# Performance work log

Measured on AMD Instinct MI355X. Metric: run time of the kernel, lower is better.

The kernel has to match this reference:

```python
import jax, jax.numpy as jnp
import numpy as np
from jax import lax


def conv2d(x, w, b, stride=1, pad=1):
    y = lax.conv_general_dilated(x, w, (stride, stride), [(pad, pad), (pad, pad)],
                                 dimension_numbers=('NCHW', 'OIHW', 'NCHW'))
    return y + b[None, :, None, None]


def nearest_resize(x, H, W):
    # torch F.interpolate(mode='nearest'): src = floor(dst * in / out)
    h, w = x.shape[-2:]
    iy = (jnp.arange(H) * h) // H
    ix = (jnp.arange(W) * w) // W
    return x[:, :, iy[:, None], ix[None, :]]


def deform_conv2d(x, offset, w, b):
    # torchvision DeformConv2d: kernel 3x3, stride 1, pad 1, dilation 1, 1 offset group
    B, C, H, W = x.shape
    K = 9
    off = offset.reshape(B, K, 2, H, W)  # per kernel tap: (dy, dx)
    dy = (jnp.arange(K) // 3 - 1).astype(x.dtype)
    dx = (jnp.arange(K) % 3 - 1).astype(x.dtype)
    yy = jnp.arange(H, dtype=x.dtype)[None, None, :, None]
    xx = jnp.arange(W, dtype=x.dtype)[None, None, None, :]
    py = yy + dy[None, :, None, None] + off[:, :, 0]  # [B,K,H,W] sample rows
    px = xx + dx[None, :, None, None] + off[:, :, 1]  # [B,K,H,W] sample cols
    y0 = jnp.floor(py)
    x0 = jnp.floor(px)
    ly = py - y0
    lx = px - x0
    y0i = y0.astype(jnp.int32)
    x0i = x0.astype(jnp.int32)
    x_flat = x.reshape(B, C, H * W)

    def gather(yi, xi, wgt):
        # zero contribution for out-of-bounds corners (torchvision zero padding)
        valid = (yi >= 0) & (yi < H) & (xi >= 0) & (xi < W)
        idx = (jnp.clip(yi, 0, H - 1) * W + jnp.clip(xi, 0, W - 1)).reshape(B, -1)
        vals = jax.vmap(lambda xf, i: xf[:, i])(x_flat, idx)  # [B, C, K*H*W]
        wv = (wgt * valid.astype(x.dtype)).reshape(B, 1, -1)
        return vals * wv

    s = gather(y0i, x0i, (1 - ly) * (1 - lx))
    s = s + gather(y0i, x0i + 1, (1 - ly) * lx)
    s = s + gather(y0i + 1, x0i, ly * (1 - lx))
    s = s + gather(y0i + 1, x0i + 1, ly * lx)
    s = s.reshape(B, C, K, H * W)  # bilinear-sampled taps
    O = w.shape[0]
    out = jnp.einsum('bckn,ock->bon', s, w.reshape(O, C, K))
    return out.reshape(B, O, H, W) + b[None, :, None, None]


def setup_inputs() -> dict:
    key = jax.random.key(0)
    ks = jax.random.split(key, 12)
    B, Ccnn, H, W = 8, 768, 28, 28
    Cvit, hv, wv = 3840, 14, 14
    d_hidn, Cout = 512, 768

    def he(k, shape):
        fan_in = shape[1] * shape[2] * shape[3]
        return jax.random.normal(k, shape, jnp.float32) * np.float32(np.sqrt(2.0 / fan_in))

    return {
        'cnn_feat': jax.random.normal(ks[0], (B, Ccnn, H, W), jnp.float32),
        'vit_feat': jax.random.normal(ks[1], (B, Cvit, hv, wv), jnp.float32),
        'w_off': he(ks[2], (18, Cvit, 3, 3)),
        'b_off': jnp.zeros((18,), jnp.float32),
        'w_def': he(ks[3], (Cout, Ccnn, 3, 3)),
        'b_def': jax.random.normal(ks[4], (Cout,), jnp.float32) * 0.01,
        'w1': he(ks[5], (d_hidn, Cout, 3, 3)),
        'b1': jax.random.normal(ks[6], (d_hidn,), jnp.float32) * 0.01,
        'w2': he(ks[7], (Cout, d_hidn, 3, 3)),
        'b2': jax.random.normal(ks[8], (Cout,), jnp.float32) * 0.01,
    }


def reference(cnn_feat, vit_feat, w_off, b_off, w_def, b_def, w1, b1, w2, b2):
    H, W = cnn_feat.shape[-2:]
    v = nearest_resize(vit_feat, H, W)
    offset = conv2d(v, w_off, b_off)                 # [B,18,H,W]
    d = deform_conv2d(cnn_feat, offset, w_def, b_def)  # [B,768,H,W]
    h = jax.nn.relu(conv2d(d, w1, b1, stride=2))     # [B,512,H/2,W/2]
    return conv2d(h, w2, b2, stride=1)               # [B,768,H/2,W/2]
```

## Files before the change

kernel.cpp:

```cpp
#include <hip/hip_runtime.h>
#include <hip/hip_bf16.h>
#include <stdint.h>

typedef __attribute__((ext_vector_type(8))) short v8s;
typedef __attribute__((ext_vector_type(4))) short v4s;
typedef __attribute__((ext_vector_type(4))) float v4f;

__device__ __forceinline__ short f2bf(float f) {
  union { float f; uint32_t u; } v; v.f = f;
  uint32_t u = v.u;
  uint32_t r = (u + 0x7fffu + ((u >> 16) & 1u)) >> 16;
  return (short)r;
}
__device__ __forceinline__ float bf2f(short s) {
  union { uint32_t u; float f; } v;
  v.u = ((uint32_t)(uint16_t)s) << 16;
  return v.f;
}
__device__ __forceinline__ void gload16(const void* g, void* l) {
  __builtin_amdgcn_global_load_lds(
      (const __attribute__((address_space(1))) void*)g,
      (__attribute__((address_space(3))) void*)l, 16, 0, 0);
}

__global__ __launch_bounds__(256) void prep_fused_k(
    const float* __restrict__ wdef, const float* __restrict__ w1,
    const float* __restrict__ w2, const float* __restrict__ woff,
    const float* __restrict__ vit, const float* __restrict__ cnn,
    short* __restrict__ wdef_p, short* __restrict__ w1_p,
    short* __restrict__ w2_p, short* __restrict__ woff2_p,
    short* __restrict__ v_t, short* __restrict__ cnn_t) {
  __shared__ float lds[32][65];
  int blk = blockIdx.x;
  int t = threadIdx.x;
  if (blk < 20736) {
    int i = blk * 256 + t;
    int e = i & 7, o = (i >> 3) % 768, p = i / (8 * 768);
    int k = p * 8 + e, tap = k / 768, c = k % 768;
    wdef_p[i] = f2bf(wdef[((size_t)o * 768 + c) * 9 + tap]);
    return;
  }
  blk -= 20736;
  if (blk < 13824) {
    int i = blk * 256 + t;
    int e = i & 7, o = (i >> 3) % 512, p = i / (8 * 512);
    int k = p * 8 + e, tap = k / 768, c = k % 768;
    w1_p[i] = f2bf(w1[((size_t)o * 768 + c) * 9 + tap]);
    return;
  }
  blk -= 13824;
  if (blk < 13824) {
    int i = blk * 256 + t;
    int e = i & 7, o = (i >> 3) % 768, p = i / (8 * 768);
    int k = p * 8 + e, tap = k / 512, c = k % 512;
    w2_p[i] = f2bf(w2[((size_t)o * 512 + c) * 9 + tap]);
    return;
  }
  blk -= 13824;
  if (blk < 2880) {
    int i = blk * 256 + t;
    int e = i & 7, m = (i >> 3) % 192, kp = i / 1536;
    int c = kp * 8 + e, o = m / 9, tap = m % 9;
    woff2_p[i] = (m < 162) ? f2bf(woff[((size_t)o * 3840 + c) * 9 + tap]) : (short)0;
    return;
  }
  blk -= 2880;
  const float* in; short* out; int C, P, bx, by;
  if (blk < 3000) { in = vit; out = v_t; C = 3840; P = 196; bx = blk % 25; by = blk / 25; }
  else { blk -= 3000; in = cnn; out = cnn_t; C = 768; P = 784; bx = blk % 98; by = blk / 98; }
  int n0 = bx * 64, c0 = by * 32;
#pragma unroll
  for (int e = 0; e < 8; e++) {
    int id = e * 256 + t;
    int cl = id >> 6, nl = id & 63;
    int n = n0 + nl;
    if (n < 8 * P) {
      int b = n / P, p = n % P;
      lds[cl][nl] = in[((size_t)b * C + c0 + cl) * P + p];
    }
  }
  __syncthreads();
  int nl = t >> 2, cs = (t & 3) * 8;
  int n = n0 + nl;
  if (n < 8 * P) {
    v8s v;
#pragma unroll
    for (int i = 0; i < 8; i++) v[i] = f2bf(lds[cs + i][nl]);
    *(v8s*)(out + (size_t)n * C + c0 + cs) = v;
  }
}

template<int MODE, int BM, int BN, int WGM, int AO, int CIN, int KSPLIT,
         int NVALID, int IH, int IW, int OW, int STRIDE, int PART>
__global__ __launch_bounds__(256) void gemm_k(const short* __restrict__ Ap,
                                              const short* __restrict__ Bp,
                                              const float* __restrict__ bias,
                                              void* __restrict__ dst,
                                              const short* __restrict__ zp) {
  constexpr int WGN = 4 / WGM;
  constexpr int WM = BM / WGM, WN = BN / WGN;
  constexpr int MF = WM / 16, NF = WN / 16;
  constexpr int CHA = BM * 8, CHT = (BM + BN) * 8;
  constexpr int NT = KSPLIT / 64;

  __shared__ __align__(16) short SM[2][CHT * 8];

  const int tid = threadIdx.x;
  const int lane = tid & 63, wid = tid >> 6;
  const int wm = wid / WGN, wn = wid % WGN;
  int bx = blockIdx.x, by = blockIdx.y;
  if constexpr (MODE == 1) {
    int bid = by * 98 + bx;
    int xcd = bid & 7, idx = bid >> 3;
    constexpr int q = 73, r = 4;
    int wg = (xcd < r ? xcd * (q + 1) : r * (q + 1) + (xcd - r) * q) + idx;
    by = wg % 6; bx = wg / 6;
  }
  const int n0 = bx * BN, m0 = by * BM;
  const int ts = blockIdx.z;
  const int kbeg = ts * KSPLIT;
  const int lrow = lane & 15, lkg = lane >> 4;

  v4f acc[MF][NF];
#pragma unroll
  for (int i = 0; i < MF; i++)
#pragma unroll
    for (int j = 0; j < NF; j++) acc[i][j] = (v4f){0.f, 0.f, 0.f, 0.f};

  auto stage = [&](int k, int buf) {
#pragma unroll
    for (int it = 0; it < CHT / 256; it++) {
      int ch = it * 256 + tid;
      const short* src;
      if (ch < CHA) {
        int kg = ch / BM, row = ch % BM;
        src = Ap + ((size_t)((k >> 3) + kg) * AO + m0 + row) * 8;
      } else {
        int bch = ch - CHA;
        int kg = bch / BN, col = bch % BN;
        int gk = k + kg * 8;
        int n = n0 + col;
        if constexpr (MODE == 0) {
          src = (n < NVALID) ? Bp + ((size_t)n * 3840 + gk) : zp;
        } else if constexpr (MODE == 1) {
          src = Bp + ((size_t)(gk >> 3) * 6272 + n) * 8;
        } else {
          int tap = gk / CIN, cc = gk % CIN;
          int b = n / (OW * OW), rem = n % (OW * OW);
          int oy = rem / OW, ox = rem % OW;
          int py = oy * STRIDE + tap / 3 - 1, px = ox * STRIDE + tap % 3 - 1;
          src = (n < NVALID && py >= 0 && py < IH && px >= 0 && px < IW)
                  ? Bp + ((size_t)((b * IH + py) * IW + px) * CIN + cc)
                  : zp;
        }
      }
      gload16(src, &SM[buf][(size_t)(it * 256 + (tid & ~63)) * 8]);
    }
  };

  stage(kbeg, 0);
  __syncthreads();
  int buf = 0;
  for (int t = 0; t < NT; ++t) {
    if (t + 1 < NT) stage(kbeg + (t + 1) * 64, buf ^ 1);
    v8s af[2][MF], bfv[2][NF];
#pragma unroll
    for (int s = 0; s < 2; s++) {
#pragma unroll
      for (int mf = 0; mf < MF; mf++)
        af[s][mf] = *(const v8s*)(&SM[buf][(size_t)((s * 4 + lkg) * BM + wm * WM + mf * 16 + lrow) * 8]);
#pragma unroll
      for (int nf = 0; nf < NF; nf++)
        bfv[s][nf] = *(const v8s*)(&SM[buf][(size_t)(CHA + (s * 4 + lkg) * BN + wn * WN + nf * 16 + lrow) * 8]);
    }
#pragma unroll
    for (int s = 0; s < 2; s++)
#pragma unroll
      for (int mf = 0; mf < MF; mf++)
#pragma unroll
        for (int nf = 0; nf < NF; nf++)
          acc[mf][nf] = __builtin_amdgcn_mfma_f32_16x16x32_bf16(af[s][mf], bfv[s][nf], acc[mf][nf], 0, 0, 0);
    __syncthreads();
    buf ^= 1;
  }

#pragma unroll
  for (int mf = 0; mf < MF; mf++) {
    int gm = m0 + wm * WM + mf * 16 + lkg * 4;
#pragma unroll
    for (int nf = 0; nf < NF; nf++) {
      int gn = n0 + wn * WN + nf * 16 + lrow;
      v4f a4 = acc[mf][nf];
      if constexpr (MODE == 0) {
        float* part = (float*)dst;
        if (gn < NVALID) {
#pragma unroll
          for (int r = 0; r < 4; r++)
            part[((size_t)ts * AO + gm + r) * 1568 + gn] = a4[r];
        }
      } else if constexpr (MODE == 1) {
        short* dt = (short*)dst;
        v4s v;
#pragma unroll
        for (int r = 0; r < 4; r++) v[r] = f2bf(a4[r] + bias[gm + r]);
        *(v4s*)(dt + (size_t)gn * 768 + gm) = v;
      } else if constexpr (MODE == 2) {
        if (gn < NVALID) {
          if constexpr (PART) {
            float* pd = (float*)dst;
            *(v4f*)(pd + ((size_t)ts * 1568 + gn) * 512 + gm) = a4;
          } else {
            short* ht = (short*)dst;
            v4s v;
#pragma unroll
            for (int r = 0; r < 4; r++) v[r] = f2bf(fmaxf(a4[r] + bias[gm + r], 0.f));
            *(v4s*)(ht + (size_t)gn * 512 + gm) = v;
          }
        }
      } else {
        if (gn < NVALID) {
          if constexpr (PART) {
            float* pd = (float*)dst;
#pragma unroll
            for (int r = 0; r < 4; r++)
              pd[((size_t)(ts * 768) + gm + r) * 1568 + gn] = a4[r];
          } else {
            float* o = (float*)dst;
            int b = gn / 196, p = gn % 196;
#pragma unroll
            for (int r = 0; r < 4; r++)
              o[((size_t)(b * 768 + gm + r)) * 196 + p] = a4[r] + bias[gm + r];
          }
        }
      }
    }
  }
}

__global__ __launch_bounds__(256) void reduce_off2_k(const float* __restrict__ part,
                                                     const float* __restrict__ boff,
                                                     float* __restrict__ offs) {
  int i = blockIdx.x * 256 + threadIdx.x;
  if (i >= 8 * 18 * 784) return;
  int b = i / (18 * 784), r = i % (18 * 784);
  int o = r / 784, yx = r % 784;
  int y = yx / 28, x = yx % 28;
  float s = boff[o];
#pragma unroll
  for (int tap = 0; tap < 9; tap++) {
    int py = y + tap / 3 - 1, px = x + tap % 3 - 1;
    if (py >= 0 && py < 28 && px >= 0 && px < 28) {
      int n = b * 196 + (py >> 1) * 14 + (px >> 1);
      int m = o * 9 + tap;
#pragma unroll
      for (int z = 0; z < 4; z++)
        s += part[((size_t)z * 192 + m) * 1568 + n];
    }
  }
  offs[i] = s;
}

__global__ __launch_bounds__(256) void reduce_c1_k(const float* __restrict__ part,
                                                   const float* __restrict__ b1,
                                                   short* __restrict__ h_t) {
  int i = blockIdx.x * 256 + threadIdx.x;
  if (i >= 1568 * 128) return;
  int n = i >> 7, o4 = (i & 127) * 4;
  v4f s0 = *(const v4f*)(part + ((size_t)n) * 512 + o4);
  v4f s1 = *(const v4f*)(part + ((size_t)(1568 + n)) * 512 + o4);
  v4f bb = *(const v4f*)(b1 + o4);
  v4s v;
#pragma unroll
  for (int r = 0; r < 4; r++) v[r] = f2bf(fmaxf(s0[r] + s1[r] + bb[r], 0.f));
  *(v4s*)(h_t + (size_t)n * 512 + o4) = v;
}

__global__ __launch_bounds__(256) void reduce_c2_k(const float* __restrict__ part,
                                                   const float* __restrict__ b2,
                                                   float* __restrict__ out) {
  int i = blockIdx.x * 256 + threadIdx.x;
  if (i >= 768 * 392) return;
  int m = i / 392, n4 = (i % 392) * 4;
  v4f s0 = *(const v4f*)(part + (size_t)m * 1568 + n4);
  v4f s1 = *(const v4f*)(part + (size_t)(768 + m) * 1568 + n4);
  float bv = b2[m];
  int b = n4 / 196, p = n4 % 196;
  v4f o;
#pragma unroll
  for (int r = 0; r < 4; r++) o[r] = s0[r] + s1[r] + bv;
  *(v4f*)(out + ((size_t)(b * 768 + m)) * 196 + p) = o;
}

__global__ __launch_bounds__(256) void sample_k(const short* __restrict__ cnn_t,
                                                const float* __restrict__ offs,
                                                short* __restrict__ sp) {
  int bid = blockIdx.x;
  int b = bid & 7;
  int r = bid >> 3;
  int tap = r >> 5;
  int rr = r & 31;
  int cg = rr >> 2, pg = rr & 3;
  int t = threadIdx.x;
  if (t >= 196) return;
  int yx = pg * 196 + t;
  int y = yx / 28, x = yx % 28;
  float dy = offs[((size_t)b * 18 + tap * 2 + 0) * 784 + yx];
  float dx = offs[((size_t)b * 18 + tap * 2 + 1) * 784 + yx];
  float py = (float)(y + tap / 3 - 1) + dy;
  float px = (float)(x + tap % 3 - 1) + dx;
  float fy = floorf(py), fx = floorf(px);
  float ly = py - fy, lx = px - fx;
  int y0 = (int)fy, x0 = (int)fx;
  int y1 = y0 + 1, x1 = x0 + 1;
  float vy0 = (y0 >= 0 && y0 < 28) ? 1.f : 0.f;
  float vy1 = (y1 >= 0 && y1 < 28) ? 1.f : 0.f;
  float vx0 = (x0 >= 0 && x0 < 28) ? 1.f : 0.f;
  float vx1 = (x1 >= 0 && x1 < 28) ? 1.f : 0.f;
  float w00 = (1.f - ly) * (1.f - lx) * vy0 * vx0;
  float w01 = (1.f - ly) * lx * vy0 * vx1;
  float w10 = ly * (1.f - lx) * vy1 * vx0;
  float w11 = ly * lx * vy1 * vx1;
  int cy0 = min(max(y0, 0), 27), cy1 = min(max(y1, 0), 27);
  int cx0 = min(max(x0, 0), 27), cx1 = min(max(x1, 0), 27);
  int c0 = cg * 12;
  const short* base = cnn_t + (size_t)b * 784 * 768 + c0 * 8;
  const short* p00 = base + (size_t)(cy0 * 28 + cx0) * 768;
  const short* p01 = base + (size_t)(cy0 * 28 + cx1) * 768;
  const short* p10 = base + (size_t)(cy1 * 28 + cx0) * 768;
  const short* p11 = base + (size_t)(cy1 * 28 + cx1) * 768;
  short* op = sp + ((size_t)(tap * 96 + c0) * 6272 + b * 784 + yx) * 8;
#pragma unroll 4
  for (int i = 0; i < 12; ++i) {
    v8s a = *(const v8s*)(p00 + i * 8);
    v8s bb = *(const v8s*)(p01 + i * 8);
    v8s c = *(const v8s*)(p10 + i * 8);
    v8s d = *(const v8s*)(p11 + i * 8);
    v8s o;
#pragma unroll
    for (int j = 0; j < 8; j++) {
      float v = w00 * bf2f(a[j]) + w01 * bf2f(bb[j]) + w10 * bf2f(c[j]) + w11 * bf2f(d[j]);
      o[j] = f2bf(v);
    }
    *(v8s*)op = o;
    op += (size_t)6272 * 8;
  }
}

extern "C" void kernel_launch(void* const* d_in, const int* in_sizes, int n_in,
                              void* d_out, int out_size, void* d_ws, size_t ws_size,
                              hipStream_t stream) {
  const float* cnn   = (const float*)d_in[0];
  const float* vit   = (const float*)d_in[1];
  const float* w_off = (const float*)d_in[2];
  const float* b_off = (const float*)d_in[3];
  const float* w_def = (const float*)d_in[4];
  const float* b_def = (const float*)d_in[5];
  const float* w1    = (const float*)d_in[6];
  const float* b1    = (const float*)d_in[7];
  const float* w2    = (const float*)d_in[8];
  const float* b2    = (const float*)d_in[9];
  float* out = (float*)d_out;
  char* ws = (char*)d_ws;

  short* wdef_p  = (short*)(ws + 0);
  short* w1_p    = (short*)(ws + 10616832);
  short* w2_p    = (short*)(ws + 17694720);
  short* woff2_p = (short*)(ws + 24772608);
  short* v_t     = (short*)(ws + 26247168);
  float* offs    = (float*)(ws + 38289408);
  float* part    = (float*)(ws + 38740992);
  short* sp      = (short*)(ws + 38740992);
  float* part1   = (float*)(ws + 38740992);
  float* part2   = (float*)(ws + 45163520);
  short* d_t     = (short*)(ws + 125445120);
  short* h_t     = (short*)(ws + 135078912);
  short* cnn_t   = (short*)(ws + 136684544);
  short* zp      = (short*)(ws + 146318336);

  hipMemsetAsync((void*)zp, 0, 256, stream);

  dim3 blk(256);
  prep_fused_k<<<56616, blk, 0, stream>>>(w_def, w1, w2, w_off, vit, cnn,
                                          wdef_p, w1_p, w2_p, woff2_p, v_t, cnn_t);

  gemm_k<0, 64, 64, 2, 192, 3840, 960, 1568, 14, 14, 14, 1, 0>
      <<<dim3(25, 3, 4), blk, 0, stream>>>(woff2_p, v_t, nullptr, part, zp);
  reduce_off2_k<<<441, blk, 0, stream>>>(part, b_off, offs);

  sample_k<<<2304, blk, 0, stream>>>(cnn_t, offs, sp);

  gemm_k<1, 128, 64, 2, 768, 768, 6912, 6272, 28, 28, 28, 1, 0>
      <<<dim3(98, 6, 1), blk, 0, stream>>>(wdef_p, sp, b_def, d_t, zp);

  gemm_k<2, 64, 64, 2, 512, 768, 3456, 1568, 28, 28, 14, 2, 1>
      <<<dim3(25, 8, 2), blk, 0, stream>>>(w1_p, d_t, b1, part1, zp);
  reduce_c1_k<<<784, blk, 0, stream>>>(part1, b1, h_t);

  gemm_k<3, 64, 64, 2, 768, 512, 2304, 1568, 14, 14, 14, 1, 1>
      <<<dim3(25, 12, 2), blk, 0, stream>>>(w2_p, h_t, b2, part2, zp);
  reduce_c2_k<<<1176, blk, 0, stream>>>(part2, b2, out);
}
```

Baseline: 287.0 us.

## Specialize deform GEMM to load A fragments directly into registers

Replaces the generic MODE-1 GEMM with a dedicated kernel. The A (weight) fragments are loaded straight from global memory into registers and double-buffered there, and only B goes through LDS, which halves LDS traffic and footprint per block. The zero-page memset is folded into the prep kernel as one extra block, removing a separate launch. The cost is more registers held for the prefetched A fragments and uncoalesced-style direct global reads of A.

Result: slower. 344.0 us (+19.9%).

```diff
diff --git a/kernel.cpp b/kernel.cpp
--- a/kernel.cpp
+++ b/kernel.cpp
@@ -29,7 +29,8 @@
     const float* __restrict__ vit, const float* __restrict__ cnn,
     short* __restrict__ wdef_p, short* __restrict__ w1_p,
     short* __restrict__ w2_p, short* __restrict__ woff2_p,
-    short* __restrict__ v_t, short* __restrict__ cnn_t) {
+    short* __restrict__ v_t, short* __restrict__ cnn_t,
+    short* __restrict__ zp) {
   __shared__ float lds[32][65];
   int blk = blockIdx.x;
   int t = threadIdx.x;
@@ -65,6 +66,10 @@
     return;
   }
   blk -= 2880;
+  if (blk >= 3000 + 2352) {
+    if (t < 128) zp[t] = 0;
+    return;
+  }
   const float* in; short* out; int C, P, bx, by;
   if (blk < 3000) { in = vit; out = v_t; C = 3840; P = 196; bx = blk % 25; by = blk / 25; }
   else { blk -= 3000; in = cnn; out = cnn_t; C = 768; P = 784; bx = blk % 98; by = blk / 98; }
@@ -87,6 +92,96 @@
 #pragma unroll
     for (int i = 0; i < 8; i++) v[i] = f2bf(lds[cs + i][nl]);
     *(v8s*)(out + (size_t)n * C + c0 + cs) = v;
+  }
+}
+
+__global__ __launch_bounds__(256) void deform_gemm_k(const short* __restrict__ Ap,
+                                                     const short* __restrict__ Bp,
+                                                     const float* __restrict__ bias,
+                                                     short* __restrict__ d_t) {
+  constexpr int NT = 108;
+  __shared__ __align__(16) short SMB[2][512 * 8];
+
+  const int tid = threadIdx.x;
+  const int lane = tid & 63, wid = tid >> 6;
+  const int wm = wid >> 1, wn = wid & 1;
+  int bid = blockIdx.y * 98 + blockIdx.x;
+  int xcd = bid & 7, idx = bid >> 3;
+  constexpr int q = 73, r = 4;
+  int wg = (xcd < r ? xcd * (q + 1) : r * (q + 1) + (xcd - r) * q) + idx;
+  const int by = wg % 6, bx = wg / 6;
+  const int n0 = bx * 64, m0 = by * 128;
+  const int lrow = lane & 15, lkg = lane >> 4;
+  const int arow = m0 + wm * 64 + lrow;
+
+  v4f acc[4][2];
+#pragma unroll
+  for (int i = 0; i < 4; i++)
+#pragma unroll
+    for (int j = 0; j < 2; j++) acc[i][j] = (v4f){0.f, 0.f, 0.f, 0.f};
+
+  v8s afA[2][4], afB[2][4];
+
+  auto loadA = [&](int k, v8s a[2][4]) {
+#pragma unroll
+    for (int s = 0; s < 2; s++)
+#pragma unroll
+      for (int mf = 0; mf < 4; mf++)
+        a[s][mf] = *(const v8s*)(Ap + ((size_t)((k >> 3) + s * 4 + lkg) * 768 + arow + mf * 16) * 8);
+  };
+  auto stageB = [&](int k, int buf) {
+#pragma unroll
+    for (int it = 0; it < 2; it++) {
+      int ch = it * 256 + tid;
+      int kg = ch >> 6, col = ch & 63;
+      gload16(Bp + ((size_t)((k >> 3) + kg) * 6272 + n0 + col) * 8,
+              &SMB[buf][(size_t)(it * 256 + (tid & ~63)) * 8]);
+    }
+  };
+  auto compute = [&](int buf, v8s a[2][4]) {
+    v8s bf[2][2];
+#pragma unroll
+    for (int s = 0; s < 2; s++)
+#pragma unroll
+      for (int nf = 0; nf < 2; nf++)
+        bf[s][nf] = *(const v8s*)(&SMB[buf][(size_t)((s * 4 + lkg) * 64 + wn * 32 + nf * 16 + lrow) * 8]);
+#pragma unroll
+    for (int s = 0; s < 2; s++)
+#pragma unroll
+      for (int mf = 0; mf < 4; mf++)
+#pragma unroll
+        for (int nf = 0; nf < 2; nf++)
+          acc[mf][nf] = __builtin_amdgcn_mfma_f32_16x16x32_bf16(a[s][mf], bf[s][nf], acc[mf][nf], 0, 0, 0);
+  };
+
+  loadA(0, afA);
+  stageB(0, 0);
+  __syncthreads();
+  for (int t = 0; t < NT; t += 2) {
+    stageB((t + 1) * 64, 1);
+    loadA((t + 1) * 64, afB);
+    compute(0, afA);
+    __syncthreads();
+    if (t + 2 < NT) {
+      stageB((t + 2) * 64, 0);
+      loadA((t + 2) * 64, afA);
+    }
+    compute(1, afB);
+    __syncthreads();
+  }
+
+#pragma unroll
+  for (int mf = 0; mf < 4; mf++) {
+    int gm = m0 + wm * 64 + mf * 16 + lkg * 4;
+#pragma unroll
+    for (int nf = 0; nf < 2; nf++) {
+      int gn = n0 + wn * 32 + nf * 16 + lrow;
+      v4f a4 = acc[mf][nf];
+      v4s v;
+#pragma unroll
+      for (int rr = 0; rr < 4; rr++) v[rr] = f2bf(a4[rr] + bias[gm + rr]);
+      *(v4s*)(d_t + (size_t)gn * 768 + gm) = v;
+    }
   }
 }
 
@@ -108,15 +203,7 @@
   const int tid = threadIdx.x;
   const int lane = tid & 63, wid = tid >> 6;
   const int wm = wid / WGN, wn = wid % WGN;
-  int bx = blockIdx.x, by = blockIdx.y;
-  if constexpr (MODE == 1) {
-    int bid = by * 98 + bx;
-    int xcd = bid & 7, idx = bid >> 3;
-    constexpr int q = 73, r = 4;
-    int wg = (xcd < r ? xcd * (q + 1) : r * (q + 1) + (xcd - r) * q) + idx;
-    by = wg % 6; bx = wg / 6;
-  }
-  const int n0 = bx * BN, m0 = by * BM;
+  const int n0 = blockIdx.x * BN, m0 = blockIdx.y * BM;
   const int ts = blockIdx.z;
   const int kbeg = ts * KSPLIT;
   const int lrow = lane & 15, lkg = lane >> 4;
@@ -142,8 +229,6 @@
         int n = n0 + col;
         if constexpr (MODE == 0) {
           src = (n < NVALID) ? Bp + ((size_t)n * 3840 + gk) : zp;
-        } else if constexpr (MODE == 1) {
-          src = Bp + ((size_t)(gk >> 3) * 6272 + n) * 8;
         } else {
           int tap = gk / CIN, cc = gk % CIN;
           int b = n / (OW * OW), rem = n % (OW * OW);
@@ -198,12 +283,6 @@
           for (int r = 0; r < 4; r++)
             part[((size_t)ts * AO + gm + r) * 1568 + gn] = a4[r];
         }
-      } else if constexpr (MODE == 1) {
-        short* dt = (short*)dst;
-        v4s v;
-#pragma unroll
-        for (int r = 0; r < 4; r++) v[r] = f2bf(a4[r] + bias[gm + r]);
-        *(v4s*)(dt + (size_t)gn * 768 + gm) = v;
       } else if constexpr (MODE == 2) {
         if (gn < NVALID) {
           if constexpr (PART) {
@@ -377,11 +456,9 @@
   short* cnn_t   = (short*)(ws + 136684544);
   short* zp      = (short*)(ws + 146318336);
 
-  hipMemsetAsync((void*)zp, 0, 256, stream);
-
   dim3 blk(256);
-  prep_fused_k<<<56616, blk, 0, stream>>>(w_def, w1, w2, w_off, vit, cnn,
-                                          wdef_p, w1_p, w2_p, woff2_p, v_t, cnn_t);
+  prep_fused_k<<<56617, blk, 0, stream>>>(w_def, w1, w2, w_off, vit, cnn,
+                                          wdef_p, w1_p, w2_p, woff2_p, v_t, cnn_t, zp);
 
   gemm_k<0, 64, 64, 2, 192, 3840, 960, 1568, 14, 14, 14, 1, 0>
       <<<dim3(25, 3, 4), blk, 0, stream>>>(woff2_p, v_t, nullptr, part, zp);
@@ -389,8 +466,7 @@
 
   sample_k<<<2304, blk, 0, stream>>>(cnn_t, offs, sp);
 
-  gemm_k<1, 128, 64, 2, 768, 768, 6912, 6272, 28, 28, 28, 1, 0>
-      <<<dim3(98, 6, 1), blk, 0, stream>>>(wdef_p, sp, b_def, d_t, zp);
+  deform_gemm_k<<<dim3(98, 6), blk, 0, stream>>>(wdef_p, sp, b_def, d_t);
 
   gemm_k<2, 64, 64, 2, 512, 768, 3456, 1568, 28, 28, 14, 2, 1>
       <<<dim3(25, 8, 2), blk, 0, stream>>>(w1_p, d_t, b1, part1, zp);
```
